# Optimization experiments

Hardware: AMD Instinct MI355X
Metric: run time of the kernel (lower is better)

## Reference

```python
import jax, jax.numpy as jnp
import numpy as np

B, N, DIM, H, DH = 2, 2048, 1024, 16, 64
INNER = H * DH
EPS = 1e-12  # F.normalize eps
MAX_LOG_SCALE = np.log(1.0 / 0.01)  # clamp max for logit_scale


def setup_inputs() -> dict:
    key = jax.random.key(0)
    k1, k2, k3, k4 = jax.random.split(key, 4)
    x = jax.random.normal(k1, (B, N, DIM), dtype=jnp.float32)
    # Linear weights stored as [in, out] (transpose of torch's [out, in])
    w_qkv = jax.random.normal(k2, (DIM, 3 * INNER), dtype=jnp.float32) * (DIM ** -0.5)
    w_out = jax.random.normal(k3, (INNER, DIM), dtype=jnp.float32) * (INNER ** -0.5)
    b_out = jax.random.normal(k4, (DIM,), dtype=jnp.float32) * 0.01
    logit_scale = jnp.full((H, 1, 1), jnp.log(10.0), dtype=jnp.float32)
    return {"x": x, "w_qkv": w_qkv, "w_out": w_out, "b_out": b_out,
            "logit_scale": logit_scale}


def reference(x, w_qkv, w_out, b_out, logit_scale):
    b, n, dim = x.shape
    h = logit_scale.shape[0]
    qkv = x @ w_qkv                              # [b, n, 3*inner]
    q, k, v = jnp.split(qkv, 3, axis=-1)
    split_heads = lambda t: t.reshape(b, n, h, -1).transpose(0, 2, 1, 3)  # b h n d
    q, k, v = split_heads(q), split_heads(k), split_heads(v)
    # L2-normalize q and k (F.normalize semantics: divide by max(norm, eps))
    qn = q / jnp.maximum(jnp.linalg.norm(q, axis=-1, keepdims=True), EPS)
    kn = k / jnp.maximum(jnp.linalg.norm(k, axis=-1, keepdims=True), EPS)
    scale = jnp.exp(jnp.minimum(logit_scale, MAX_LOG_SCALE))  # [h,1,1], per-head temp
    cos_dots = jnp.einsum('bhid,bhjd->bhij', qn, kn) * scale   # [b,h,n,n]
    # NOTE: masking in the source mutates the unused plain-dot `dots` tensor,
    # so the output never depends on the mask -> faithfully omitted.
    attn = jax.nn.softmax(cos_dots, axis=-1)
    out = jnp.einsum('bhij,bhjd->bhid', attn, v)               # [b,h,n,d]
    out = out.transpose(0, 2, 1, 3).reshape(b, n, -1)          # [b,n,inner]
    return out @ w_out + b_out
```

## Files before the change

kernel.cpp:

```cpp
#include <hip/hip_runtime.h>

typedef __attribute__((ext_vector_type(8))) short bf16x8;
typedef __attribute__((ext_vector_type(4))) float f32x4;
typedef __attribute__((ext_vector_type(16))) float f32x16;
typedef unsigned short u16;
typedef unsigned int u32;
typedef __attribute__((ext_vector_type(4))) unsigned int u32x4;

#define DEV static __device__ __forceinline__

DEV u16 f2bf(float f) {
  u32 u = __float_as_uint(f);
  u += 0x7FFFu + ((u >> 16) & 1u);
  return (u16)(u >> 16);
}
DEV float bf2f(u16 h) { return __uint_as_float(((u32)h) << 16); }

DEV void gload16(const void* g, void* l) {
  __builtin_amdgcn_global_load_lds((const __attribute__((address_space(1))) void*)g,
                                   (__attribute__((address_space(3))) void*)l, 16, 0, 0);
}

#define MFMA16(a, b, c) __builtin_amdgcn_mfma_f32_16x16x32_bf16((a), (b), (c), 0, 0, 0)
#define MFMA32(a, b, c) __builtin_amdgcn_mfma_f32_32x32x16_bf16((a), (b), (c), 0, 0, 0)

DEV u32 cvtpk(float lo, float hi) {
  u32 r;
  asm("v_cvt_pk_bf16_f32 %0, %1, %2" : "=v"(r) : "v"(lo), "v"(hi));
  return r;
}
DEV void plswap(u32& a, u32& b) {
  asm volatile("v_permlane32_swap_b32 %0, %1" : "+v"(a), "+v"(b));
}
DEV bf16x8 asbf(u32x4 v) {
  union { u32x4 u; bf16x8 b; } x;
  x.u = v;
  return x.b;
}

DEV void rawbar() {
  __builtin_amdgcn_sched_barrier(0);
  asm volatile("" ::: "memory");
  __builtin_amdgcn_s_barrier();
  asm volatile("" ::: "memory");
  __builtin_amdgcn_sched_barrier(0);
}
#define VMCNT4() asm volatile("s_waitcnt vmcnt(4)" ::: "memory")
#define VMCNT0() asm volatile("s_waitcnt vmcnt(0)" ::: "memory")
#define LGKM0()  asm volatile("s_waitcnt lgkmcnt(0)" ::: "memory")

#define MAXLOG 4.6051701859880914f

__global__ __launch_bounds__(256) void k_prep(const float* __restrict__ x,
                                              u16* __restrict__ Xbf,
                                              const float* __restrict__ w_qkv,
                                              u16* __restrict__ Wqkvt,
                                              const float* __restrict__ w_out,
                                              u16* __restrict__ Woutt) {
  __shared__ u16 lds[64][72];
  int blk = blockIdx.x;
  int t = threadIdx.x;
  if (blk < 2048) {
    int i = blk * 256 + t;
    const f32x4* p = (const f32x4*)(x + (size_t)i * 8);
    f32x4 a = p[0], b = p[1];
    bf16x8 o;
    o[0] = (short)f2bf(a[0]); o[1] = (short)f2bf(a[1]);
    o[2] = (short)f2bf(a[2]); o[3] = (short)f2bf(a[3]);
    o[4] = (short)f2bf(b[0]); o[5] = (short)f2bf(b[1]);
    o[6] = (short)f2bf(b[2]); o[7] = (short)f2bf(b[3]);
    *(bf16x8*)(Xbf + (size_t)i * 8) = o;
    return;
  }
  const float* src;
  u16* dst;
  int rows, cols, bx, by;
  if (blk < 2816) {
    int q = blk - 2048;
    src = w_qkv; dst = Wqkvt; rows = 1024; cols = 3072;
    bx = q % 48; by = q / 48;
  } else {
    int q = blk - 2816;
    src = w_out; dst = Woutt; rows = 1024; cols = 1024;
    bx = q % 16; by = q / 16;
  }
  int r0 = by * 64, c0 = bx * 64;
  int r = t >> 2, cq = (t & 3) << 4;
  const float* s = src + (size_t)(r0 + r) * cols + c0 + cq;
#pragma unroll
  for (int i = 0; i < 16; i += 4) {
    f32x4 v = *(const f32x4*)(s + i);
    lds[r][cq + i + 0] = f2bf(v[0]);
    lds[r][cq + i + 1] = f2bf(v[1]);
    lds[r][cq + i + 2] = f2bf(v[2]);
    lds[r][cq + i + 3] = f2bf(v[3]);
  }
  __syncthreads();
  int c = t >> 2, rq = (t & 3) << 4;
  bf16x8 o0, o1;
#pragma unroll
  for (int i = 0; i < 8; ++i) o0[i] = (short)lds[rq + i][c];
#pragma unroll
  for (int i = 0; i < 8; ++i) o1[i] = (short)lds[rq + 8 + i][c];
  u16* d = dst + (size_t)(c0 + c) * rows + r0 + rq;
  *(bf16x8*)d = o0;
  *(bf16x8*)(d + 8) = o1;
}

__global__ __launch_bounds__(256) void k_gemm_qkv(const u16* __restrict__ A,
                                                  const u16* __restrict__ Bt,
                                                  const float* __restrict__ logit_scale,
                                                  u16* __restrict__ Qn, u16* __restrict__ Kn,
                                                  u16* __restrict__ Vt,
                                                  int M, int N, int K, int nbx) {
  __shared__ __align__(16) u16 lsA[128 * 32];
  __shared__ __align__(16) u16 lsB[128 * 32];
  int tid = threadIdx.x;
  int lane = tid & 63, wave = tid >> 6;
  int wr = (wave >> 1) * 64, wc = (wave & 1) * 64;
  int nwg = gridDim.x;
  int orig = blockIdx.x;
  int wg = (orig & 7) * (nwg >> 3) + (orig >> 3);
  int bm = (wg / nbx) * 128, bn = (wg % nbx) * 128;

  f32x4 acc[4][4] = {};

  const u16* aSrc[2]; u16* aDst[2];
  const u16* bSrc[2]; u16* bDst[2];
#pragma unroll
  for (int j = 0; j < 2; ++j) {
    int s = wave * 128 + j * 64 + lane;
    int row = s >> 2, chunk = s & 3;
    int g = chunk ^ ((row >> 1) & 3);
    aSrc[j] = A + (size_t)(bm + row) * K + g * 8;
    bSrc[j] = Bt + (size_t)(bn + row) * K + g * 8;
    aDst[j] = &lsA[(wave * 128 + j * 64) * 8];
    bDst[j] = &lsB[(wave * 128 + j * 64) * 8];
  }

  for (int k0 = 0; k0 < K; k0 += 32) {
    __syncthreads();
    gload16(aSrc[0] + k0, aDst[0]);
    gload16(aSrc[1] + k0, aDst[1]);
    gload16(bSrc[0] + k0, bDst[0]);
    gload16(bSrc[1] + k0, bDst[1]);
    __syncthreads();
    bf16x8 af[4], bfr[4];
#pragma unroll
    for (int m = 0; m < 4; ++m) {
      int r = wr + m * 16 + (lane & 15);
      int p = (lane >> 4) ^ ((r >> 1) & 3);
      af[m] = *(const bf16x8*)&lsA[r * 32 + p * 8];
    }
#pragma unroll
    for (int n = 0; n < 4; ++n) {
      int r = wc + n * 16 + (lane & 15);
      int p = (lane >> 4) ^ ((r >> 1) & 3);
      bfr[n] = *(const bf16x8*)&lsB[r * 32 + p * 8];
    }
#pragma unroll
    for (int m = 0; m < 4; ++m)
#pragma unroll
      for (int n = 0; n < 4; ++n)
        acc[m][n] = MFMA16(af[m], bfr[n], acc[m][n]);
  }

  int colg = bn + wc;
  if (colg < 2048) {
    bool isQ = colg < 1024;
    int h = (colg >> 6) & 15;
    float scale = isQ ? __expf(fminf(logit_scale[h], MAXLOG)) : 1.0f;
    u16* dst = isQ ? Qn : Kn;
#pragma unroll
    for (int m = 0; m < 4; ++m) {
#pragma unroll
      for (int j = 0; j < 4; ++j) {
        float ss = 0.f;
#pragma unroll
        for (int n = 0; n < 4; ++n) ss += acc[m][n][j] * acc[m][n][j];
        ss += __shfl_xor(ss, 1, 64);
        ss += __shfl_xor(ss, 2, 64);
        ss += __shfl_xor(ss, 4, 64);
        ss += __shfl_xor(ss, 8, 64);
        float r = scale / fmaxf(sqrtf(ss), 1e-12f);
        int row = bm + wr + m * 16 + ((lane >> 4) << 2) + j;
        int b = row >> 11, tok = row & 2047;
        size_t base = ((size_t)(b * 16 + h) * 2048 + tok) * 64;
#pragma unroll
        for (int n = 0; n < 4; ++n)
          dst[base + n * 16 + (lane & 15)] = f2bf(acc[m][n][j] * r);
      }
    }
  } else {
    int h = ((colg - 2048) >> 6) & 15;
    __syncthreads();
    u16* sl = (wave < 2 ? lsA : lsB) + (wave & 1) * 2048;
    int bb = bm >> 11, bmm = bm & 2047;
    size_t vbase = ((size_t)(bb * 16 + h) * 64) * 2048;
#pragma unroll
    for (int rr = 0; rr < 2; ++rr) {
#pragma unroll
      for (int nn = 0; nn < 2; ++nn) {
        int n = rr * 2 + nn;
        int d32 = nn * 16 + (lane & 15);
        int xr = (d32 & 7) << 3;
#pragma unroll
        for (int m = 0; m < 4; ++m)
#pragma unroll
          for (int j = 0; j < 4; ++j) {
            int tok = m * 16 + ((lane >> 4) << 2) + j;
            sl[d32 * 64 + (tok ^ xr)] = f2bf(acc[m][n][j]);
          }
      }
      LGKM0();
#pragma unroll
      for (int ri = 0; ri < 4; ++ri) {
        int li = ri * 64 + lane;
        int d32 = li >> 3, c = li & 7;
        int cx = c ^ (d32 & 7);
        bf16x8 v = *(const bf16x8*)&sl[d32 * 64 + cx * 8];
        size_t dsto = vbase + (size_t)(rr * 32 + d32) * 2048 + bmm + wr + c * 8;
        *(bf16x8*)&Vt[dsto] = v;
      }
      LGKM0();
    }
  }
}

__global__ __launch_bounds__(256) void k_gemm_out(const u16* __restrict__ A,
                                                  const u16* __restrict__ Bt,
                                                  float* __restrict__ Cout,
                                                  const float* __restrict__ bias,
                                                  int M, int N, int K, int nbx) {
  __shared__ __align__(16) u16 lsA[128 * 32];
  __shared__ __align__(16) u16 lsB[64 * 32];
  int tid = threadIdx.x;
  int lane = tid & 63, wave = tid >> 6;
  int wr = (wave >> 1) * 64, wc = (wave & 1) * 32;
  int nwg = gridDim.x;
  int orig = blockIdx.x;
  int wg = (orig & 7) * (nwg >> 3) + (orig >> 3);
  int bm = (wg / nbx) * 128, bn = (wg % nbx) * 64;

  f32x4 acc[4][2] = {};

  const u16* aSrc[2]; u16* aDst[2];
  const u16* bSrc;    u16* bDst;
#pragma unroll
  for (int j = 0; j < 2; ++j) {
    int s = wave * 128 + j * 64 + lane;
    int row = s >> 2, chunk = s & 3;
    int g = chunk ^ ((row >> 1) & 3);
    aSrc[j] = A + (size_t)(bm + row) * K + g * 8;
    aDst[j] = &lsA[(wave * 128 + j * 64) * 8];
  }
  {
    int s = wave * 64 + lane;
    int row = s >> 2, chunk = s & 3;
    int g = chunk ^ ((row >> 1) & 3);
    bSrc = Bt + (size_t)(bn + row) * K + g * 8;
    bDst = &lsB[(wave * 64) * 8];
  }

  for (int k0 = 0; k0 < K; k0 += 32) {
    __syncthreads();
    gload16(aSrc[0] + k0, aDst[0]);
    gload16(aSrc[1] + k0, aDst[1]);
    gload16(bSrc + k0, bDst);
    __syncthreads();
    bf16x8 af[4], bfr[2];
#pragma unroll
    for (int m = 0; m < 4; ++m) {
      int r = wr + m * 16 + (lane & 15);
      int p = (lane >> 4) ^ ((r >> 1) & 3);
      af[m] = *(const bf16x8*)&lsA[r * 32 + p * 8];
    }
#pragma unroll
    for (int n = 0; n < 2; ++n) {
      int r = wc + n * 16 + (lane & 15);
      int p = (lane >> 4) ^ ((r >> 1) & 3);
      bfr[n] = *(const bf16x8*)&lsB[r * 32 + p * 8];
    }
#pragma unroll
    for (int m = 0; m < 4; ++m)
#pragma unroll
      for (int n = 0; n < 2; ++n)
        acc[m][n] = MFMA16(af[m], bfr[n], acc[m][n]);
  }

#pragma unroll
  for (int m = 0; m < 4; ++m) {
    int row = bm + wr + m * 16 + ((lane >> 4) << 2);
#pragma unroll
    for (int n = 0; n < 2; ++n) {
      int col = bn + wc + n * 16 + (lane & 15);
      float bb = bias[col];
#pragma unroll
      for (int j = 0; j < 4; ++j)
        Cout[(size_t)(row + j) * N + col] = acc[m][n][j] + bb;
    }
  }
}

__global__ __launch_bounds__(256, 2) void k_flash(const u16* __restrict__ Qn,
                                                  const u16* __restrict__ Kn,
                                                  const u16* __restrict__ Vt,
                                                  const float* __restrict__ logit_scale,
                                                  u16* __restrict__ AO) {
  __shared__ __align__(16) u16 lsK[2][64 * 64];
  __shared__ __align__(16) u16 lsV[2][64 * 64];
  __shared__ float l_s[4][32];
  int tid = threadIdx.x, lane = tid & 63, wave = tid >> 6;
  int r31 = lane & 31, h = lane >> 5;
  int bh = blockIdx.x, b = bh >> 4, hd = bh & 15;
  int qw = blockIdx.y * 128 + wave * 32;
  const u16* Q = Qn + (size_t)bh * 2048 * 64;
  const u16* Kb = Kn + (size_t)bh * 2048 * 64;
  const u16* Vb = Vt + (size_t)bh * 64 * 2048;

  float negC = -__expf(fminf(logit_scale[hd], MAXLOG));

  bf16x8 qB[4];
#pragma unroll
  for (int ks = 0; ks < 4; ++ks)
    qB[ks] = *(const bf16x8*)&Q[(size_t)(qw + r31) * 64 + ks * 16 + h * 8];

  size_t kGO[2], vGO[2];
  int lOff[2];
#pragma unroll
  for (int j = 0; j < 2; ++j) {
    int s = j * 256 + tid;
    int row = s >> 3, ch = s & 7, g = ch ^ (row & 7);
    kGO[j] = (size_t)row * 64 + g * 8;
    vGO[j] = (size_t)row * 2048 + g * 8;
    lOff[j] = s * 8;
  }

  int off[2][4];
#pragma unroll
  for (int a = 0; a < 2; ++a)
#pragma unroll
    for (int ks = 0; ks < 4; ++ks)
      off[a][ks] = (a * 32 + r31) * 64 + ((((ks << 1) | h) ^ (r31 & 7)) << 3);

  f32x16 o0, o1;
#pragma unroll
  for (int i = 0; i < 16; ++i) { o0[i] = 0.f; o1[i] = 0.f; }
  float lsm[4] = {0.f, 0.f, 0.f, 0.f};

#define STAGE(dstbuf, kvt)                                          \
  {                                                                 \
    size_t kv0 = (size_t)(kvt) * 64;                                \
    gload16(Kb + kv0 * 64 + kGO[0], &lsK[dstbuf][lOff[0]]);         \
    gload16(Kb + kv0 * 64 + kGO[1], &lsK[dstbuf][lOff[1]]);         \
    gload16(Vb + kv0 + vGO[0], &lsV[dstbuf][lOff[0]]);              \
    gload16(Vb + kv0 + vGO[1], &lsV[dstbuf][lOff[1]]);              \
  }

  STAGE(0, 0);

#pragma unroll 1
  for (int t = 0; t < 32; ++t) {
    int cur = t & 1;
    if (t < 31) {
      STAGE(cur ^ 1, t + 1);
      VMCNT4();
    } else {
      VMCNT0();
    }
    rawbar();
    const u16* Kl = lsK[cur];
    const u16* Vl = lsV[cur];

    f32x16 s0, s1;
#pragma unroll
    for (int i = 0; i < 16; ++i) { s0[i] = negC; s1[i] = negC; }
    bf16x8 k0f[4], k1f[4];
#pragma unroll
    for (int ks = 0; ks < 4; ++ks) {
      k0f[ks] = *(const bf16x8*)&Kl[off[0][ks]];
      k1f[ks] = *(const bf16x8*)&Kl[off[1][ks]];
    }
    __builtin_amdgcn_s_setprio(1);
#pragma unroll
    for (int ks = 0; ks < 4; ++ks) {
      s0 = MFMA32(k0f[ks], qB[ks], s0);
      s1 = MFMA32(k1f[ks], qB[ks], s1);
    }
    __builtin_amdgcn_s_setprio(0);

    bf16x8 v0f[4], v1f[4];
#pragma unroll
    for (int ks = 0; ks < 4; ++ks) {
      v0f[ks] = *(const bf16x8*)&Vl[off[0][ks]];
      v1f[ks] = *(const bf16x8*)&Vl[off[1][ks]];
    }

#pragma unroll
    for (int i = 0; i < 16; ++i) {
      float e0 = __expf(s0[i]);
      float e1 = __expf(s1[i]);
      lsm[i & 3] += e0 + e1;
      s0[i] = e0; s1[i] = e1;
    }

    bf16x8 pa[4];
    {
      u32 c0 = cvtpk(s0[0], s0[1]),  c1 = cvtpk(s0[2], s0[3]);
      u32 c2 = cvtpk(s0[4], s0[5]),  c3 = cvtpk(s0[6], s0[7]);
      u32 c4 = cvtpk(s0[8], s0[9]),  c5 = cvtpk(s0[10], s0[11]);
      u32 c6 = cvtpk(s0[12], s0[13]), c7 = cvtpk(s0[14], s0[15]);
      plswap(c0, c2); plswap(c1, c3); plswap(c4, c6); plswap(c5, c7);
      pa[0] = asbf((u32x4){c0, c1, c2, c3});
      pa[1] = asbf((u32x4){c4, c5, c6, c7});
      u32 d0 = cvtpk(s1[0], s1[1]),  d1 = cvtpk(s1[2], s1[3]);
      u32 d2 = cvtpk(s1[4], s1[5]),  d3 = cvtpk(s1[6], s1[7]);
      u32 d4 = cvtpk(s1[8], s1[9]),  d5 = cvtpk(s1[10], s1[11]);
      u32 d6 = cvtpk(s1[12], s1[13]), d7 = cvtpk(s1[14], s1[15]);
      plswap(d0, d2); plswap(d1, d3); plswap(d4, d6); plswap(d5, d7);
      pa[2] = asbf((u32x4){d0, d1, d2, d3});
      pa[3] = asbf((u32x4){d4, d5, d6, d7});
    }

    __builtin_amdgcn_s_setprio(1);
#pragma unroll
    for (int ks = 0; ks < 4; ++ks) {
      o0 = MFMA32(pa[ks], v0f[ks], o0);
      o1 = MFMA32(pa[ks], v1f[ks], o1);
    }
    __builtin_amdgcn_s_setprio(0);

    rawbar();
  }
#undef STAGE

  float lsum = (lsm[0] + lsm[1]) + (lsm[2] + lsm[3]);
  float ltot = lsum + __shfl_xor(lsum, 32, 64);
  if (h == 0) l_s[wave][r31] = 1.0f / ltot;
  __syncthreads();

#pragma unroll
  for (int r = 0; r < 16; ++r) {
    int cr = (r & 3) + ((r >> 2) << 3) + (h << 2);
    int qr = qw + cr;
    float li = l_s[wave][cr];
    size_t base = ((size_t)(b * 2048 + qr)) * 1024 + hd * 64;
    AO[base + r31] = f2bf(o0[r] * li);
    AO[base + 32 + r31] = f2bf(o1[r] * li);
  }
}

extern "C" void kernel_launch(void* const* d_in, const int* in_sizes, int n_in,
                              void* d_out, int out_size, void* d_ws, size_t ws_size,
                              hipStream_t stream) {
  const float* x = (const float*)d_in[0];
  const float* w_qkv = (const float*)d_in[1];
  const float* w_out = (const float*)d_in[2];
  const float* b_out = (const float*)d_in[3];
  const float* logit_scale = (const float*)d_in[4];

  char* ws = (char*)d_ws;
  u16* Xbf   = (u16*)(ws);
  u16* Wqkvt = (u16*)(ws + (8ll << 20));
  u16* Woutt = (u16*)(ws + (14ll << 20));
  u16* Qn    = (u16*)(ws + (16ll << 20));
  u16* Kn    = (u16*)(ws + (24ll << 20));
  u16* Vt    = (u16*)(ws + (32ll << 20));
  u16* AO    = Xbf;
  float* out = (float*)d_out;

  k_prep<<<3072, 256, 0, stream>>>(x, Xbf, w_qkv, Wqkvt, w_out, Woutt);
  k_gemm_qkv<<<768, 256, 0, stream>>>(Xbf, Wqkvt, logit_scale, Qn, Kn, Vt,
                                      4096, 3072, 1024, 24);
  k_flash<<<dim3(32, 16), 256, 0, stream>>>(Qn, Kn, Vt, logit_scale, AO);
  k_gemm_out<<<512, 256, 0, stream>>>(AO, Woutt, out, b_out,
                                      4096, 1024, 1024, 16);
}
```

Baseline: 117.0 us.

## Double-buffer LDS tiles in QKV and output GEMMs to overlap loads with MFMA

Both projection GEMMs now keep two LDS buffers and issue the global-to-LDS loads for the next K tile before computing on the current one. Explicit vmcnt waits and raw barriers replace the two __syncthreads per iteration. The aim is to hide global load latency behind MFMA work. In exchange, LDS use doubles, the K loop is hardcoded to 32 iterations (K=1024), and correctness now depends on the manual waitcnt accounting.

```diff
diff --git a/kernel.cpp b/kernel.cpp
--- a/kernel.cpp
+++ b/kernel.cpp
@@ -46,6 +46,7 @@
   __builtin_amdgcn_sched_barrier(0);
 }
 #define VMCNT4() asm volatile("s_waitcnt vmcnt(4)" ::: "memory")
+#define VMCNT3() asm volatile("s_waitcnt vmcnt(3)" ::: "memory")
 #define VMCNT0() asm volatile("s_waitcnt vmcnt(0)" ::: "memory")
 #define LGKM0()  asm volatile("s_waitcnt lgkmcnt(0)" ::: "memory")
 
@@ -113,8 +114,8 @@
                                                   u16* __restrict__ Qn, u16* __restrict__ Kn,
                                                   u16* __restrict__ Vt,
                                                   int M, int N, int K, int nbx) {
-  __shared__ __align__(16) u16 lsA[128 * 32];
-  __shared__ __align__(16) u16 lsB[128 * 32];
+  __shared__ __align__(16) u16 lsA[2][128 * 32];
+  __shared__ __align__(16) u16 lsB[2][128 * 32];
   int tid = threadIdx.x;
   int lane = tid & 63, wave = tid >> 6;
   int wr = (wave >> 1) * 64, wc = (wave & 1) * 64;
@@ -125,8 +126,9 @@
 
   f32x4 acc[4][4] = {};
 
-  const u16* aSrc[2]; u16* aDst[2];
-  const u16* bSrc[2]; u16* bDst[2];
+  const u16* aSrc[2];
+  const u16* bSrc[2];
+  int lOf[2];
 #pragma unroll
   for (int j = 0; j < 2; ++j) {
     int s = wave * 128 + j * 64 + lane;
@@ -134,36 +136,51 @@
     int g = chunk ^ ((row >> 1) & 3);
     aSrc[j] = A + (size_t)(bm + row) * K + g * 8;
     bSrc[j] = Bt + (size_t)(bn + row) * K + g * 8;
-    aDst[j] = &lsA[(wave * 128 + j * 64) * 8];
-    bDst[j] = &lsB[(wave * 128 + j * 64) * 8];
-  }
-
-  for (int k0 = 0; k0 < K; k0 += 32) {
-    __syncthreads();
-    gload16(aSrc[0] + k0, aDst[0]);
-    gload16(aSrc[1] + k0, aDst[1]);
-    gload16(bSrc[0] + k0, bDst[0]);
-    gload16(bSrc[1] + k0, bDst[1]);
-    __syncthreads();
+    lOf[j] = s * 8;
+  }
+
+#define STAGEG(B, T)                                        \
+  {                                                         \
+    int kk = (T) * 32;                                      \
+    gload16(aSrc[0] + kk, &lsA[B][lOf[0]]);                 \
+    gload16(aSrc[1] + kk, &lsA[B][lOf[1]]);                 \
+    gload16(bSrc[0] + kk, &lsB[B][lOf[0]]);                 \
+    gload16(bSrc[1] + kk, &lsB[B][lOf[1]]);                 \
+  }
+
+  STAGEG(0, 0);
+
+#pragma unroll 1
+  for (int t = 0; t < 32; ++t) {
+    int cur = t & 1;
+    if (t < 31) {
+      STAGEG(cur ^ 1, t + 1);
+      VMCNT4();
+    } else {
+      VMCNT0();
+    }
+    rawbar();
     bf16x8 af[4], bfr[4];
 #pragma unroll
     for (int m = 0; m < 4; ++m) {
       int r = wr + m * 16 + (lane & 15);
       int p = (lane >> 4) ^ ((r >> 1) & 3);
-      af[m] = *(const bf16x8*)&lsA[r * 32 + p * 8];
+      af[m] = *(const bf16x8*)&lsA[cur][r * 32 + p * 8];
     }
 #pragma unroll
     for (int n = 0; n < 4; ++n) {
       int r = wc + n * 16 + (lane & 15);
       int p = (lane >> 4) ^ ((r >> 1) & 3);
-      bfr[n] = *(const bf16x8*)&lsB[r * 32 + p * 8];
+      bfr[n] = *(const bf16x8*)&lsB[cur][r * 32 + p * 8];
     }
 #pragma unroll
     for (int m = 0; m < 4; ++m)
 #pragma unroll
       for (int n = 0; n < 4; ++n)
         acc[m][n] = MFMA16(af[m], bfr[n], acc[m][n]);
-  }
+    rawbar();
+  }
+#undef STAGEG
 
   int colg = bn + wc;
   if (colg < 2048) {
@@ -194,7 +211,7 @@
   } else {
     int h = ((colg - 2048) >> 6) & 15;
     __syncthreads();
-    u16* sl = (wave < 2 ? lsA : lsB) + (wave & 1) * 2048;
+    u16* sl = (wave < 2 ? &lsA[0][0] : &lsB[0][0]) + (wave & 1) * 2048;
     int bb = bm >> 11, bmm = bm & 2047;
     size_t vbase = ((size_t)(bb * 16 + h) * 64) * 2048;
 #pragma unroll
@@ -232,8 +249,8 @@
                                                   float* __restrict__ Cout,
                                                   const float* __restrict__ bias,
                                                   int M, int N, int K, int nbx) {
-  __shared__ __align__(16) u16 lsA[128 * 32];
-  __shared__ __align__(16) u16 lsB[64 * 32];
+  __shared__ __align__(16) u16 lsA[2][128 * 32];
+  __shared__ __align__(16) u16 lsB[2][64 * 32];
   int tid = threadIdx.x;
   int lane = tid & 63, wave = tid >> 6;
   int wr = (wave >> 1) * 64, wc = (wave & 1) * 32;
@@ -244,49 +261,66 @@
 
   f32x4 acc[4][2] = {};
 
-  const u16* aSrc[2]; u16* aDst[2];
-  const u16* bSrc;    u16* bDst;
+  const u16* aSrc[2];
+  const u16* bSrc;
+  int lOfA[2], lOfB;
 #pragma unroll
   for (int j = 0; j < 2; ++j) {
     int s = wave * 128 + j * 64 + lane;
     int row = s >> 2, chunk = s & 3;
     int g = chunk ^ ((row >> 1) & 3);
     aSrc[j] = A + (size_t)(bm + row) * K + g * 8;
-    aDst[j] = &lsA[(wave * 128 + j * 64) * 8];
+    lOfA[j] = s * 8;
   }
   {
     int s = wave * 64 + lane;
     int row = s >> 2, chunk = s & 3;
     int g = chunk ^ ((row >> 1) & 3);
     bSrc = Bt + (size_t)(bn + row) * K + g * 8;
-    bDst = &lsB[(wave * 64) * 8];
-  }
-
-  for (int k0 = 0; k0 < K; k0 += 32) {
-    __syncthreads();
-    gload16(aSrc[0] + k0, aDst[0]);
-    gload16(aSrc[1] + k0, aDst[1]);
-    gload16(bSrc + k0, bDst);
-    __syncthreads();
+    lOfB = s * 8;
+  }
+
+#define STAGEO(B, T)                                        \
+  {                                                         \
+    int kk = (T) * 32;                                      \
+    gload16(aSrc[0] + kk, &lsA[B][lOfA[0]]);                \
+    gload16(aSrc[1] + kk, &lsA[B][lOfA[1]]);                \
+    gload16(bSrc + kk, &lsB[B][lOfB]);                      \
+  }
+
+  STAGEO(0, 0);
+
+#pragma unroll 1
+  for (int t = 0; t < 32; ++t) {
+    int cur = t & 1;
+    if (t < 31) {
+      STAGEO(cur ^ 1, t + 1);
+      VMCNT3();
+    } else {
+      VMCNT0();
+    }
+    rawbar();
     bf16x8 af[4], bfr[2];
 #pragma unroll
     for (int m = 0; m < 4; ++m) {
       int r = wr + m * 16 + (lane & 15);
       int p = (lane >> 4) ^ ((r >> 1) & 3);
-      af[m] = *(const bf16x8*)&lsA[r * 32 + p * 8];
+      af[m] = *(const bf16x8*)&lsA[cur][r * 32 + p * 8];
     }
 #pragma unroll
     for (int n = 0; n < 2; ++n) {
       int r = wc + n * 16 + (lane & 15);
       int p = (lane >> 4) ^ ((r >> 1) & 3);
-      bfr[n] = *(const bf16x8*)&lsB[r * 32 + p * 8];
+      bfr[n] = *(const bf16x8*)&lsB[cur][r * 32 + p * 8];
     }
 #pragma unroll
     for (int m = 0; m < 4; ++m)
 #pragma unroll
       for (int n = 0; n < 2; ++n)
         acc[m][n] = MFMA16(af[m], bfr[n], acc[m][n]);
-  }
+    rawbar();
+  }
+#undef STAGEO
 
 #pragma unroll
   for (int m = 0; m < 4; ++m) {
```

After: 122.9 us. 1.05x slower.
